# Kernel optimization log

Measured on AMD Instinct MI355X. Metric: run time of the kernel, lower is better.

The kernel has to match this reference:

```python
import jax, jax.numpy as jnp
import numpy as np

# MORR all-pass ring parameters (MORRConfig_20um defaults: attenuation / self-coupling)
A_MORR = 0.8578
R_MORR = 0.8578
KS = 3       # kernel_size
MB = 8       # miniblock (circulant block size)
BN_EPS = 1e-5


def mrr_roundtrip_phase_to_tr(phi):
    # through-port transmission of an all-pass microring vs roundtrip phase
    c = jnp.cos(phi)
    num = A_MORR * A_MORR - 2.0 * A_MORR * R_MORR * c + R_MORR * R_MORR
    den = 1.0 - 2.0 * A_MORR * R_MORR * c + (A_MORR * R_MORR) ** 2
    return num / den


def setup_inputs() -> dict:
    key = jax.random.key(0)
    k1, k2 = jax.random.split(key, 2)
    B, C, H, W = 64, 64, 32, 32
    outC = 64
    q = (C * KS * KS + MB - 1) // MB   # grid_dim_x = 72
    p = (outC + MB - 1) // MB          # grid_dim_y = 8
    x = jax.random.normal(k1, (B, C, H, W), jnp.float32)
    weight = jax.random.normal(k2, (p, q, MB), jnp.float32) * 0.05  # circulant eigen-vectors per block
    gamma = jnp.ones((outC,), jnp.float32)   # BatchNorm2d weight
    beta = jnp.zeros((outC,), jnp.float32)   # BatchNorm2d bias
    return {"x": x, "weight": weight, "gamma": gamma, "beta": beta}


def reference(x, weight, gamma, beta):
    B, C, H, W = x.shape
    p, q, mb = weight.shape
    outC = gamma.shape[0]
    Ho, Wo = H, W  # stride=1, padding=1, ks=3
    L = Ho * Wo
    # im2col (torch F.unfold ordering: C major, then kh, kw)
    xp = jnp.pad(x, ((0, 0), (0, 0), (1, 1), (1, 1)))
    cols = jnp.stack([xp[:, :, i:i + Ho, j:j + Wo]
                      for i in range(KS) for j in range(KS)], axis=2)  # [B,C,9,Ho,Wo]
    cols = cols.reshape(B, C * KS * KS, L).transpose(0, 2, 1)          # [B,L,C*k*k]
    assert C * KS * KS == q * mb, "patch dim must pad to q*mb"
    s = cols.reshape(B, L, q, mb)
    s = s * s  # optical intensity (power) fed into the MORR
    # block-circulant weight: Wc[p,q,i,j] = weight[p,q,(i-j) mod mb]
    i_idx = jnp.arange(mb)
    idx = (i_idx[:, None] - i_idx[None, :]) % mb
    Wc = weight[:, :, idx]                                             # [p,q,mb,mb]
    # accumulated roundtrip phase per output node
    phase = jnp.einsum('blqj,pqij->blpi', s, Wc)                       # [B,L,p,mb]
    tr = mrr_roundtrip_phase_to_tr(phase)
    out = tr.reshape(B, L, p * mb)[:, :, :outC]                        # truncate to out_channel
    out = out.transpose(0, 2, 1).reshape(B, outC, Ho, Wo)
    # BatchNorm2d (training mode: batch statistics) + Hardtanh(-1, 1)
    mean = out.mean(axis=(0, 2, 3), keepdims=True)
    var = out.var(axis=(0, 2, 3), keepdims=True)
    y = (out - mean) * jax.lax.rsqrt(var + BN_EPS)
    y = y * gamma[None, :, None, None] + beta[None, :, None, None]
    return jnp.clip(y, -1.0, 1.0)
```

## Files before the change

kernel.cpp:

```cpp
#include <hip/hip_runtime.h>
#include <hip/hip_cooperative_groups.h>

namespace cg = cooperative_groups;


#define A_MORR 0.8578f
#define R_MORR 0.8578f
#define TR_C1 (A_MORR * A_MORR + R_MORR * R_MORR)
#define TR_C2 (-2.0f * A_MORR * R_MORR)
#define TR_C3 (1.0f + (A_MORR * R_MORR) * (A_MORR * R_MORR))
#define BN_EPS 1e-5f

#define NPIX 65536
#define X2_LO 26112
#define SMEM_BYTES 52224

typedef __attribute__((ext_vector_type(8))) short bf16x8;
typedef __attribute__((ext_vector_type(16))) float f32x16;

__device__ __forceinline__ void bf16split(float s, unsigned short& h, unsigned short& l) {
    union { float f; unsigned u; } cv; cv.f = s;
    unsigned r = (cv.u + 0x7fffu + ((cv.u >> 16) & 1u)) & 0xffff0000u;
    h = (unsigned short)(r >> 16);
    union { unsigned u; float f; } hv; hv.u = r;
    float lo = s - hv.f;
    cv.f = lo;
    unsigned r2 = cv.u + 0x7fffu + ((cv.u >> 16) & 1u);
    l = (unsigned short)(r2 >> 16);
}

__global__ __launch_bounds__(256) void prep_kernel(const float* __restrict__ w,
                                                   char* __restrict__ wfrag,
                                                   float* __restrict__ stats) {
    int gtid = blockIdx.x * 256 + threadIdx.x;
    if (gtid < 128) stats[gtid] = 0.0f;
    if (gtid < 36864) {
        int j    = gtid & 7;
        int lane = (gtid >> 3) & 63;
        int okm  = gtid >> 9;
        int mt   = okm & 1;
        int ks   = (okm >> 1) & 3;
        int off  = okm >> 3;
        int oc   = mt * 32 + (lane & 31);
        int c    = ks * 16 + (lane >> 5) * 8 + j;
        int kg   = c * 9 + off;
        float val = w[(oc >> 3) * 576 + (kg >> 3) * 8 + ((oc - kg) & 7)];
        unsigned short h, l;
        bf16split(val, h, l);
        ((unsigned short*)(wfrag + okm * 2048))[lane * 8 + j] = h;
        ((unsigned short*)(wfrag + okm * 2048 + 1024))[lane * 8 + j] = l;
    }
}

template <int FUSED>
__global__ __launch_bounds__(512, 4) void conv_kernel(const float* __restrict__ x,
                                                      const char* __restrict__ wfrag,
                                                      float* __restrict__ out,
                                                      float* __restrict__ stats,
                                                      const float* __restrict__ gamma,
                                                      const float* __restrict__ beta) {
    const int rt  = blockIdx.x;
    const int b   = blockIdx.y;
    const int tid = threadIdx.x;

    __shared__ __align__(16) char smem[SMEM_BYTES];

    if (tid < 192) {
        int prec = tid & 1;
        int g    = (tid >> 1) & 7;
        int rc   = tid >> 4;
        int r    = rc >> 1;
        int c    = (rc & 1) ? 33 : 0;
        *(uint4*)(smem + prec * X2_LO + ((r * 34 + c) << 7) + (g << 4)) = uint4{0, 0, 0, 0};
    }

    {
        const int rh  = tid & 1;
        const int co  = (tid >> 1) & 7;
        const int chp = tid >> 4;
        const float* xb = x + (size_t)(b * 64 + 2 * chp) * 1024;
#pragma unroll
        for (int r3 = 0; r3 < 3; ++r3) {
            int rr = rh * 3 + r3;
            int gr = rt * 4 - 1 + rr;
            float4 a0 = {0.f, 0.f, 0.f, 0.f}, a1 = {0.f, 0.f, 0.f, 0.f};
            if (gr >= 0 && gr < 32) {
                const float* rp = xb + gr * 32 + co * 4;
                a0 = *(const float4*)rp;
                a1 = *(const float4*)(rp + 1024);
            }
            float s0[4] = {a0.x * a0.x, a0.y * a0.y, a0.z * a0.z, a0.w * a0.w};
            float s1[4] = {a1.x * a1.x, a1.y * a1.y, a1.z * a1.z, a1.w * a1.w};
#pragma unroll
            for (int i = 0; i < 4; ++i) {
                unsigned short h0, l0, h1, l1;
                bf16split(s0[i], h0, l0);
                bf16split(s1[i], h1, l1);
                int c    = 1 + co * 4 + i;
                int base = ((rr * 34 + c) << 7) + (((chp >> 2) ^ (c & 7)) << 4)
                         + ((chp & 3) << 2);
                *(unsigned*)(smem + base)         = (unsigned)h0 | ((unsigned)h1 << 16);
                *(unsigned*)(smem + X2_LO + base) = (unsigned)l0 | ((unsigned)l1 << 16);
            }
        }
    }
    __syncthreads();

    const int lane = tid & 63;
    const int wv   = tid >> 6;
    const int wmt  = wv & 1;
    const int kh   = (wv >> 1) & 1;
    const int py   = wv >> 2;
    const int col  = lane & 31;
    const int hs   = lane >> 5;
    const int rowb = py * 2;

    f32x16 acc0, acc1;
#pragma unroll
    for (int i = 0; i < 16; ++i) { acc0[i] = 0.f; acc1[i] = 0.f; }

    const char* wbase = wfrag + wmt * 2048 + (size_t)lane * 16;

#pragma unroll
    for (int dj = 0; dj < 3; ++dj) {
        const int c  = col + dj;
        const int c7 = c & 7;
#pragma unroll
        for (int ksi = 0; ksi < 2; ++ksi) {
            const int ks = kh * 2 + ksi;
            const int g  = ((ks * 2 + hs) ^ c7) << 4;
            bf16x8 bh[4], bl[4];
#pragma unroll
            for (int rr = 0; rr < 4; ++rr) {
                const char* sp = smem + (((rowb + rr) * 34 + c) << 7) + g;
                bh[rr] = *(const bf16x8*)sp;
                bl[rr] = *(const bf16x8*)(sp + X2_LO);
            }
#pragma unroll
            for (int di = 0; di < 3; ++di) {
                const char* wp = wbase + (di * 3 + dj) * 16384 + ks * 4096;
                bf16x8 ah = *(const bf16x8*)wp;
                bf16x8 al = *(const bf16x8*)(wp + 1024);
                acc0 = __builtin_amdgcn_mfma_f32_32x32x16_bf16(ah, bh[di],     acc0, 0, 0, 0);
                acc1 = __builtin_amdgcn_mfma_f32_32x32x16_bf16(ah, bh[di + 1], acc1, 0, 0, 0);
                acc0 = __builtin_amdgcn_mfma_f32_32x32x16_bf16(ah, bl[di],     acc0, 0, 0, 0);
                acc1 = __builtin_amdgcn_mfma_f32_32x32x16_bf16(ah, bl[di + 1], acc1, 0, 0, 0);
                acc0 = __builtin_amdgcn_mfma_f32_32x32x16_bf16(al, bh[di],     acc0, 0, 0, 0);
                acc1 = __builtin_amdgcn_mfma_f32_32x32x16_bf16(al, bh[di + 1], acc1, 0, 0, 0);
            }
        }
    }

    float* mergef = (float*)smem;
    __syncthreads();
    {
        const int slot = (wmt * 2 + py) * 2;
        if (kh == 1) {
#pragma unroll
            for (int r = 0; r < 16; ++r) {
                mergef[((slot + 0) * 16 + r) * 64 + lane] = acc0[r];
                mergef[((slot + 1) * 16 + r) * 64 + lane] = acc1[r];
            }
        }
        __syncthreads();
        if (kh == 0) {
#pragma unroll
            for (int r = 0; r < 16; ++r) {
                float p0 = acc0[r] + mergef[((slot + 0) * 16 + r) * 64 + lane];
                float p1 = acc1[r] + mergef[((slot + 1) * 16 + r) * 64 + lane];
                float c0 = __cosf(p0);
                float c1 = __cosf(p1);
                acc0[r] = fmaf(TR_C2, c0, TR_C1) / fmaf(TR_C2, c0, TR_C3);
                acc1[r] = fmaf(TR_C2, c1, TR_C1) / fmaf(TR_C2, c1, TR_C3);
            }
        }
    }
    __syncthreads();

    float* red1 = mergef;
    float* red2 = red1 + 64 * 66;
    if (kh == 0) {
#pragma unroll
        for (int r = 0; r < 16; ++r) {
            int ocl  = (r & 3) + 8 * (r >> 2) + 4 * hs;
            float t0 = acc0[r], t1 = acc1[r];
            int ri = (wmt * 32 + ocl) * 66 + py * 32 + col;
            red1[ri] = t0 + t1;
            red2[ri] = t0 * t0 + t1 * t1;
        }
    }
    __syncthreads();
    if (tid < 64) {
        float s1 = 0.f, s2 = 0.f;
#pragma unroll
        for (int q = 0; q < 64; ++q) {
            s1 += red1[tid * 66 + q];
            s2 += red2[tid * 66 + q];
        }
        atomicAdd(&stats[tid], s1);
        atomicAdd(&stats[64 + tid], s2);
    }

    if constexpr (FUSED) {
        cg::this_grid().sync();
        float* ssc = red2 + 64 * 66;
        float* ssh = ssc + 64;
        if (tid < 64) {
            float s1 = __hip_atomic_load(&stats[tid], __ATOMIC_RELAXED, __HIP_MEMORY_SCOPE_AGENT);
            float s2 = __hip_atomic_load(&stats[64 + tid], __ATOMIC_RELAXED, __HIP_MEMORY_SCOPE_AGENT);
            const float invN = 1.0f / (float)NPIX;
            float mean = s1 * invN;
            float var  = s2 * invN - mean * mean;
            float sc   = gamma[tid] * rsqrtf(var + BN_EPS);
            ssc[tid] = sc;
            ssh[tid] = beta[tid] - mean * sc;
        }
        __syncthreads();
        if (kh == 0) {
            const size_t outbase = ((size_t)b * 64 + wmt * 32) * 1024 + rt * 128;
#pragma unroll
            for (int r = 0; r < 16; ++r) {
                int ocl  = (r & 3) + 8 * (r >> 2) + 4 * hs;
                float sc = ssc[wmt * 32 + ocl];
                float sh = ssh[wmt * 32 + ocl];
                float y0 = fminf(1.0f, fmaxf(-1.0f, fmaf(acc0[r], sc, sh)));
                float y1 = fminf(1.0f, fmaxf(-1.0f, fmaf(acc1[r], sc, sh)));
                size_t o = outbase + (size_t)ocl * 1024 + py * 64 + col;
                out[o]      = y0;
                out[o + 32] = y1;
            }
        }
    } else {
        if (kh == 0) {
            const size_t outbase = ((size_t)b * 64 + wmt * 32) * 1024 + rt * 128;
#pragma unroll
            for (int r = 0; r < 16; ++r) {
                int ocl  = (r & 3) + 8 * (r >> 2) + 4 * hs;
                size_t o = outbase + (size_t)ocl * 1024 + py * 64 + col;
                out[o]      = acc0[r];
                out[o + 32] = acc1[r];
            }
        }
    }
}

__global__ __launch_bounds__(64) void stats_kernel(const float* __restrict__ stats,
                                                   const float* __restrict__ gamma,
                                                   const float* __restrict__ beta,
                                                   float* __restrict__ ss) {
    int oc = threadIdx.x;
    if (oc >= 64) return;
    const float invN = 1.0f / (float)NPIX;
    float mean = stats[oc] * invN;
    float var  = stats[64 + oc] * invN - mean * mean;
    float sc   = gamma[oc] * rsqrtf(var + BN_EPS);
    ss[oc]      = sc;
    ss[64 + oc] = beta[oc] - mean * sc;
}

__global__ __launch_bounds__(256) void norm_kernel(float* __restrict__ out,
                                                   const float* __restrict__ ss) {
    int i = blockIdx.x * 256 + threadIdx.x;
    float4 v = ((float4*)out)[i];
    int oc = (i >> 8) & 63;
    float sc = ss[oc];
    float sh = ss[64 + oc];
    v.x = fminf(1.0f, fmaxf(-1.0f, fmaf(v.x, sc, sh)));
    v.y = fminf(1.0f, fmaxf(-1.0f, fmaf(v.y, sc, sh)));
    v.z = fminf(1.0f, fmaxf(-1.0f, fmaf(v.z, sc, sh)));
    v.w = fminf(1.0f, fmaxf(-1.0f, fmaf(v.w, sc, sh)));
    ((float4*)out)[i] = v;
}

extern "C" void kernel_launch(void* const* d_in, const int* in_sizes, int n_in,
                              void* d_out, int out_size, void* d_ws, size_t ws_size,
                              hipStream_t stream) {
    const float* x     = (const float*)d_in[0];
    const float* w     = (const float*)d_in[1];
    const float* gamma = (const float*)d_in[2];
    const float* beta  = (const float*)d_in[3];
    float* out = (float*)d_out;

    char*  wfrag = (char*)d_ws;
    float* stats = (float*)((char*)d_ws + 147456);
    float* ss    = stats + 128;

    hipLaunchKernelGGL(prep_kernel, dim3(144), dim3(256), 0, stream, w, wfrag, stats);

    int maxb = 0;
    hipError_t qe = hipOccupancyMaxActiveBlocksPerMultiprocessor(
        &maxb, reinterpret_cast<const void*>(&conv_kernel<1>), 512, 0);
    bool fused = (qe == hipSuccess) && (maxb >= 2);

    if (fused) {
        void* cargs[] = { (void*)&x, (void*)&wfrag, (void*)&out,
                          (void*)&stats, (void*)&gamma, (void*)&beta };
        hipError_t le = hipLaunchCooperativeKernel(
            reinterpret_cast<const void*>(&conv_kernel<1>),
            dim3(8, 64), dim3(512), cargs, 0, stream);
        if (le != hipSuccess) fused = false;
    }
    if (!fused) {
        hipLaunchKernelGGL(conv_kernel<0>, dim3(8, 64), dim3(512), 0, stream,
                           x, wfrag, out, stats, gamma, beta);
        hipLaunchKernelGGL(stats_kernel, dim3(1), dim3(64), 0, stream, stats, gamma, beta, ss);
        hipLaunchKernelGGL(norm_kernel, dim3(4096), dim3(256), 0, stream, out, ss);
    }
}
```

Before: 48.97 us.

## Replace cooperative grid sync with per-block partials and separate stats/normalize kernels

Drops the cooperative launch and grid-wide barrier, along with the atomic accumulation of the batch-norm sums. Each conv block now writes its per-channel partial sums to a workspace array. A 64-block stats kernel reduces those partials and a separate normalize pass applies BN and hardtanh. This removes atomics and grid-sync stalls and lowers the launch-bounds occupancy hint to 2, at the cost of extra launches and a full extra read/write pass over the output.

After: 42.00 us. 1.17x faster.

```diff
diff --git a/kernel.cpp b/kernel.cpp
--- a/kernel.cpp
+++ b/kernel.cpp
@@ -1,7 +1,4 @@
 #include <hip/hip_runtime.h>
-#include <hip/hip_cooperative_groups.h>
-
-namespace cg = cooperative_groups;
 
 
 #define A_MORR 0.8578f
@@ -14,6 +11,7 @@
 #define NPIX 65536
 #define X2_LO 26112
 #define SMEM_BYTES 52224
+#define NBLK 512
 
 typedef __attribute__((ext_vector_type(8))) short bf16x8;
 typedef __attribute__((ext_vector_type(16))) float f32x16;
@@ -30,10 +28,8 @@
 }
 
 __global__ __launch_bounds__(256) void prep_kernel(const float* __restrict__ w,
-                                                   char* __restrict__ wfrag,
-                                                   float* __restrict__ stats) {
+                                                   char* __restrict__ wfrag) {
     int gtid = blockIdx.x * 256 + threadIdx.x;
-    if (gtid < 128) stats[gtid] = 0.0f;
     if (gtid < 36864) {
         int j    = gtid & 7;
         int lane = (gtid >> 3) & 63;
@@ -52,15 +48,13 @@
     }
 }
 
-template <int FUSED>
-__global__ __launch_bounds__(512, 4) void conv_kernel(const float* __restrict__ x,
+__global__ __launch_bounds__(512, 2) void conv_kernel(const float* __restrict__ x,
                                                       const char* __restrict__ wfrag,
                                                       float* __restrict__ out,
-                                                      float* __restrict__ stats,
-                                                      const float* __restrict__ gamma,
-                                                      const float* __restrict__ beta) {
+                                                      float* __restrict__ partials) {
     const int rt  = blockIdx.x;
     const int b   = blockIdx.y;
+    const int bid = b * 8 + rt;
     const int tid = threadIdx.x;
 
     __shared__ __align__(16) char smem[SMEM_BYTES];
@@ -197,65 +191,48 @@
             s1 += red1[tid * 66 + q];
             s2 += red2[tid * 66 + q];
         }
-        atomicAdd(&stats[tid], s1);
-        atomicAdd(&stats[64 + tid], s2);
-    }
-
-    if constexpr (FUSED) {
-        cg::this_grid().sync();
-        float* ssc = red2 + 64 * 66;
-        float* ssh = ssc + 64;
-        if (tid < 64) {
-            float s1 = __hip_atomic_load(&stats[tid], __ATOMIC_RELAXED, __HIP_MEMORY_SCOPE_AGENT);
-            float s2 = __hip_atomic_load(&stats[64 + tid], __ATOMIC_RELAXED, __HIP_MEMORY_SCOPE_AGENT);
-            const float invN = 1.0f / (float)NPIX;
-            float mean = s1 * invN;
-            float var  = s2 * invN - mean * mean;
-            float sc   = gamma[tid] * rsqrtf(var + BN_EPS);
-            ssc[tid] = sc;
-            ssh[tid] = beta[tid] - mean * sc;
+        partials[(size_t)tid * NBLK + bid]        = s1;
+        partials[(size_t)(64 + tid) * NBLK + bid] = s2;
+    }
+
+    if (kh == 0) {
+        const size_t outbase = ((size_t)b * 64 + wmt * 32) * 1024 + rt * 128;
+#pragma unroll
+        for (int r = 0; r < 16; ++r) {
+            int ocl  = (r & 3) + 8 * (r >> 2) + 4 * hs;
+            size_t o = outbase + (size_t)ocl * 1024 + py * 64 + col;
+            out[o]      = acc0[r];
+            out[o + 32] = acc1[r];
+        }
+    }
+}
+
+__global__ __launch_bounds__(512) void stats_kernel(const float* __restrict__ partials,
+                                                    const float* __restrict__ gamma,
+                                                    const float* __restrict__ beta,
+                                                    float* __restrict__ ss) {
+    const int c   = blockIdx.x;
+    const int tid = threadIdx.x;
+    __shared__ float r1[512], r2[512];
+    r1[tid] = partials[(size_t)c * NBLK + tid];
+    r2[tid] = partials[(size_t)(64 + c) * NBLK + tid];
+    __syncthreads();
+#pragma unroll
+    for (int s = 256; s > 0; s >>= 1) {
+        if (tid < s) {
+            r1[tid] += r1[tid + s];
+            r2[tid] += r2[tid + s];
         }
         __syncthreads();
-        if (kh == 0) {
-            const size_t outbase = ((size_t)b * 64 + wmt * 32) * 1024 + rt * 128;
-#pragma unroll
-            for (int r = 0; r < 16; ++r) {
-                int ocl  = (r & 3) + 8 * (r >> 2) + 4 * hs;
-                float sc = ssc[wmt * 32 + ocl];
-                float sh = ssh[wmt * 32 + ocl];
-                float y0 = fminf(1.0f, fmaxf(-1.0f, fmaf(acc0[r], sc, sh)));
-                float y1 = fminf(1.0f, fmaxf(-1.0f, fmaf(acc1[r], sc, sh)));
-                size_t o = outbase + (size_t)ocl * 1024 + py * 64 + col;
-                out[o]      = y0;
-                out[o + 32] = y1;
-            }
-        }
-    } else {
-        if (kh == 0) {
-            const size_t outbase = ((size_t)b * 64 + wmt * 32) * 1024 + rt * 128;
-#pragma unroll
-            for (int r = 0; r < 16; ++r) {
-                int ocl  = (r & 3) + 8 * (r >> 2) + 4 * hs;
-                size_t o = outbase + (size_t)ocl * 1024 + py * 64 + col;
-                out[o]      = acc0[r];
-                out[o + 32] = acc1[r];
-            }
-        }
-    }
-}
-
-__global__ __launch_bounds__(64) void stats_kernel(const float* __restrict__ stats,
-                                                   const float* __restrict__ gamma,
-                                                   const float* __restrict__ beta,
-                                                   float* __restrict__ ss) {
-    int oc = threadIdx.x;
-    if (oc >= 64) return;
-    const float invN = 1.0f / (float)NPIX;
-    float mean = stats[oc] * invN;
-    float var  = stats[64 + oc] * invN - mean * mean;
-    float sc   = gamma[oc] * rsqrtf(var + BN_EPS);
-    ss[oc]      = sc;
-    ss[64 + oc] = beta[oc] - mean * sc;
+    }
+    if (tid == 0) {
+        const float invN = 1.0f / (float)NPIX;
+        float mean = r1[0] * invN;
+        float var  = r2[0] * invN - mean * mean;
+        float sc   = gamma[c] * rsqrtf(var + BN_EPS);
+        ss[c]      = sc;
+        ss[64 + c] = beta[c] - mean * sc;
+    }
 }
 
 __global__ __launch_bounds__(256) void norm_kernel(float* __restrict__ out,
@@ -281,29 +258,12 @@
     const float* beta  = (const float*)d_in[3];
     float* out = (float*)d_out;
 
-    char*  wfrag = (char*)d_ws;
-    float* stats = (float*)((char*)d_ws + 147456);
-    float* ss    = stats + 128;
-
-    hipLaunchKernelGGL(prep_kernel, dim3(144), dim3(256), 0, stream, w, wfrag, stats);
-
-    int maxb = 0;
-    hipError_t qe = hipOccupancyMaxActiveBlocksPerMultiprocessor(
-        &maxb, reinterpret_cast<const void*>(&conv_kernel<1>), 512, 0);
-    bool fused = (qe == hipSuccess) && (maxb >= 2);
-
-    if (fused) {
-        void* cargs[] = { (void*)&x, (void*)&wfrag, (void*)&out,
-                          (void*)&stats, (void*)&gamma, (void*)&beta };
-        hipError_t le = hipLaunchCooperativeKernel(
-            reinterpret_cast<const void*>(&conv_kernel<1>),
-            dim3(8, 64), dim3(512), cargs, 0, stream);
-        if (le != hipSuccess) fused = false;
-    }
-    if (!fused) {
-        hipLaunchKernelGGL(conv_kernel<0>, dim3(8, 64), dim3(512), 0, stream,
-                           x, wfrag, out, stats, gamma, beta);
-        hipLaunchKernelGGL(stats_kernel, dim3(1), dim3(64), 0, stream, stats, gamma, beta, ss);
-        hipLaunchKernelGGL(norm_kernel, dim3(4096), dim3(256), 0, stream, out, ss);
-    }
-}
+    char*  wfrag    = (char*)d_ws;
+    float* partials = (float*)((char*)d_ws + 147456);
+    float* ss       = partials + 128 * NBLK;
+
+    hipLaunchKernelGGL(prep_kernel, dim3(144), dim3(256), 0, stream, w, wfrag);
+    hipLaunchKernelGGL(conv_kernel, dim3(8, 64), dim3(512), 0, stream, x, wfrag, out, partials);
+    hipLaunchKernelGGL(stats_kernel, dim3(64), dim3(512), 0, stream, partials, gamma, beta, ss);
+    hipLaunchKernelGGL(norm_kernel, dim3(4096), dim3(256), 0, stream, out, ss);
+}
```
